# Performance work log

Hardware: AMD Instinct MI355X
Metric: run time of the kernel (lower is better)

The kernel has to match this reference:

```python
import jax, jax.numpy as jnp
import numpy as np

N, F_IN, HID, NCLS, E = 50000, 128, 256, 40, 600000
BN_EPS = 1e-5


def setup_inputs() -> dict:
    key = jax.random.key(0)
    ks = jax.random.split(key, 12)
    x = jax.random.normal(ks[0], (N, F_IN), dtype=jnp.float32)
    edge_index = jax.random.randint(ks[1], (2, E), 0, N, dtype=jnp.int64)
    # BatchNorm0 (over input features) running stats + affine params
    bn0_gamma = jnp.ones((F_IN,), jnp.float32)
    bn0_beta = jnp.zeros((F_IN,), jnp.float32)
    bn0_mean = jax.random.normal(ks[2], (F_IN,), jnp.float32) * 0.1
    bn0_var = jax.random.uniform(ks[3], (F_IN,), jnp.float32, 0.5, 1.5)
    # GINConv1 linear: F_IN -> HID
    W1 = jax.random.normal(ks[4], (F_IN, HID), jnp.float32) / np.sqrt(F_IN)
    b1 = jnp.zeros((HID,), jnp.float32)
    # BatchNorm1 (over hidden)
    bn1_gamma = jnp.ones((HID,), jnp.float32)
    bn1_beta = jnp.zeros((HID,), jnp.float32)
    bn1_mean = jax.random.normal(ks[5], (HID,), jnp.float32) * 0.1
    bn1_var = jax.random.uniform(ks[6], (HID,), jnp.float32, 0.5, 1.5)
    # GINConv2 linear: HID -> NCLS
    W2 = jax.random.normal(ks[7], (HID, NCLS), jnp.float32) / np.sqrt(HID)
    b2 = jnp.zeros((NCLS,), jnp.float32)
    return {
        "x": x, "edge_index": edge_index,
        "bn0_gamma": bn0_gamma, "bn0_beta": bn0_beta,
        "bn0_mean": bn0_mean, "bn0_var": bn0_var,
        "W1": W1, "b1": b1,
        "bn1_gamma": bn1_gamma, "bn1_beta": bn1_beta,
        "bn1_mean": bn1_mean, "bn1_var": bn1_var,
        "W2": W2, "b2": b2,
    }


def _bn_eval(h, gamma, beta, mean, var):
    return (h - mean) * (gamma / jnp.sqrt(var + BN_EPS)) + beta


def _gin_agg(h, src, dst, n):
    # sum_{j in N(i)} h_j  (scatter-add over edges), plus self term (eps=0)
    return h + jax.ops.segment_sum(h[src], dst, num_segments=n)


def reference(x, edge_index, bn0_gamma, bn0_beta, bn0_mean, bn0_var,
              W1, b1, bn1_gamma, bn1_beta, bn1_mean, bn1_var, W2, b2):
    # Eval mode: dropout / dropout_edge are identity; BN uses running stats.
    src, dst = edge_index[0], edge_index[1]
    n = x.shape[0]
    h = _bn_eval(x, bn0_gamma, bn0_beta, bn0_mean, bn0_var)
    h = _gin_agg(h, src, dst, n) @ W1 + b1          # GINConv1
    h = _bn_eval(h, bn1_gamma, bn1_beta, bn1_mean, bn1_var)
    h = jax.nn.relu(h)
    out = _gin_agg(h, src, dst, n) @ W2 + b2        # GINConv2 -> logits [N, NCLS]
    return out
```

## Files before the change

kernel.cpp:

```cpp
#include <hip/hip_runtime.h>

#define NN 50000
#define FIN 128
#define HID 256
#define NCLS 40
#define NE 600000
#define BN_EPS 1e-5f
#define MAXDEG 64
#define GSTR 64
#define NSLICE 6250
#define NFILLB 4688
#define NCONVB 6250

typedef _Float16 half4_t __attribute__((ext_vector_type(4)));
typedef _Float16 half8_t __attribute__((ext_vector_type(8)));
typedef float float2_t __attribute__((ext_vector_type(2)));
typedef float float4_t __attribute__((ext_vector_type(4)));


#define OFF_DEG    1600000
#define OFF_GH     1664000
#define OFF_XQ     3264000
#define OFF_W1T    4864000
#define OFF_W2T    4880384
#define OFF_P      4886528
#define OFF_Q      4886784

__global__ void prep_convert_fill_k(const float* __restrict__ W1, const float* __restrict__ W2,
                                    const float* __restrict__ bn0_g, const float* __restrict__ bn0_b,
                                    const float* __restrict__ bn0_m, const float* __restrict__ bn0_v,
                                    const float* __restrict__ b1,
                                    const float* __restrict__ bn1_g, const float* __restrict__ bn1_b,
                                    const float* __restrict__ bn1_m, const float* __restrict__ bn1_v,
                                    _Float16* __restrict__ W1T, _Float16* __restrict__ W2T,
                                    float* __restrict__ p, float* __restrict__ q,
                                    const float4* __restrict__ x4, unsigned int* __restrict__ xq,
                                    const int* __restrict__ ei, int* __restrict__ deg,
                                    unsigned short* __restrict__ pad) {
    int t = threadIdx.x;
    int b = blockIdx.x;
    if (b >= 9) {
        int fb = b - 9;
        if (fb < NFILLB) {
            int grp = fb >> 3;
            int slice = fb & 7;
            int ebase = grp * 1024 + t;
            #pragma unroll
            for (int k = 0; k < 4; ++k) {
                int e = ebase + k * 256;
                if (e < NE) {
                    int dst = ei[NE + e];
                    if (dst / NSLICE == slice) {
                        int src = ei[e];
                        int pos = atomicAdd(&deg[dst], 1);
                        if (pos < MAXDEG) pad[(size_t)dst * MAXDEG + pos] = (unsigned short)src;
                    }
                }
            }
        } else {
            int i = (fb - NFILLB) * 256 + t;
            if (i < NN * 32) {
                float4 v = x4[i];
                int r = 0;
                r = __builtin_amdgcn_cvt_pk_fp8_f32(v.x, v.y, r, false);
                r = __builtin_amdgcn_cvt_pk_fp8_f32(v.z, v.w, r, true);
                xq[i] = (unsigned int)r;
            }
        }
        return;
    }
    if (b < 8) {
        __shared__ _Float16 T[64][65];
        __shared__ float s0l[64], s1l[64];
        int k0 = (b >> 2) * 64;
        int c0 = (b & 3) * 64;
        if (t < 64) {
            s0l[t] = bn0_g[k0 + t] * rsqrtf(bn0_v[k0 + t] + BN_EPS);
        } else if (t < 128) {
            int c = t - 64;
            s1l[c] = bn1_g[c0 + c] * rsqrtf(bn1_v[c0 + c] + BN_EPS);
        }
        __syncthreads();
        int cc = t & 63;
        #pragma unroll
        for (int i = 0; i < 16; ++i) {
            int idx = i * 256 + t;
            int kk = idx >> 6;
            T[cc][kk] = (_Float16)(W1[(size_t)(k0 + kk) * HID + c0 + cc] * s0l[kk] * s1l[cc]);
        }
        __syncthreads();
        #pragma unroll
        for (int i = 0; i < 16; ++i) {
            int idx = i * 256 + t;
            int c2 = idx >> 6, kk2 = idx & 63;
            W1T[(size_t)(c0 + c2) * FIN + k0 + kk2] = T[c2][kk2];
        }
    } else {
        __shared__ float t0s[FIN];
        if (t < FIN) {
            float s = bn0_g[t] * rsqrtf(bn0_v[t] + BN_EPS);
            t0s[t] = bn0_b[t] - bn0_m[t] * s;
        }
        float sc = bn1_g[t] * rsqrtf(bn1_v[t] + BN_EPS);
        __syncthreads();
        float v = 0.f;
        for (int k = 0; k < FIN; ++k) v += t0s[k] * W1[(size_t)k * HID + t];
        p[t] = v * sc;
        q[t] = (b1[t] - bn1_m[t]) * sc + bn1_b[t];
        for (int c = 0; c < 48; ++c) {
            float w = (c < NCLS) ? W2[(size_t)t * NCLS + c] : 0.f;
            W2T[(size_t)c * HID + t] = (_Float16)w;
        }
    }
}

#define FP8ACC(v)                                                          \
    {                                                                      \
        float2_t f0 = __builtin_amdgcn_cvt_pk_f32_fp8((int)(v).x, false);  \
        float2_t f1 = __builtin_amdgcn_cvt_pk_f32_fp8((int)(v).x, true);   \
        float2_t f2 = __builtin_amdgcn_cvt_pk_f32_fp8((int)(v).y, false);  \
        float2_t f3 = __builtin_amdgcn_cvt_pk_f32_fp8((int)(v).y, true);   \
        ax0 += f0[0]; ax1 += f0[1]; ax2 += f1[0]; ax3 += f1[1];            \
        ax4 += f2[0]; ax5 += f2[1]; ax6 += f3[0]; ax7 += f3[1];            \
    }

__launch_bounds__(256, 6)
__global__ void gather_gemm_k(const uint2* __restrict__ xq, const int* __restrict__ deg,
                              const unsigned short* __restrict__ pad,
                              const _Float16* __restrict__ W1T, const _Float16* __restrict__ W2T,
                              const float* __restrict__ p, const float* __restrict__ q,
                              _Float16* __restrict__ gh) {
    __shared__ _Float16 smem[32 * 264];
    __shared__ float scdeg[32];
    int t = threadIdx.x;
    int w = t >> 6, lane = t & 63;
    int l16 = lane & 15;
    int qw = lane >> 4;
    int sbase = lane & 48;
    int node_base = blockIdx.x * 32;

    for (int pr = 0; pr < 2; ++pr) {
        int ln = w * 8 + pr * 4 + qw;
        int n = node_base + ln;
        float ax0 = 0.f, ax1 = 0.f, ax2 = 0.f, ax3 = 0.f;
        float ax4 = 0.f, ax5 = 0.f, ax6 = 0.f, ax7 = 0.f;
        int dcnt = 0;
        if (n < NN) {
            int d = deg[n];
            dcnt = d < MAXDEG ? d : MAXDEG;
            uint2 sv = xq[(size_t)n * 16 + l16];
            FP8ACC(sv);
        }
        int base = 0;
        while (base < dcnt) {
            int cnt = dcnt - base;
            if (cnt > 16) cnt = 16;
            int vi = (l16 < cnt) ? (int)pad[(size_t)n * MAXDEG + base + l16] : 0;
            int j = 0;
            for (; j + 7 < cnt; j += 8) {
                int s0 = __shfl(vi, sbase + j),     s1 = __shfl(vi, sbase + j + 1);
                int s2 = __shfl(vi, sbase + j + 2), s3 = __shfl(vi, sbase + j + 3);
                int s4 = __shfl(vi, sbase + j + 4), s5 = __shfl(vi, sbase + j + 5);
                int s6 = __shfl(vi, sbase + j + 6), s7 = __shfl(vi, sbase + j + 7);
                uint2 v0 = xq[(size_t)s0 * 16 + l16];
                uint2 v1 = xq[(size_t)s1 * 16 + l16];
                uint2 v2 = xq[(size_t)s2 * 16 + l16];
                uint2 v3 = xq[(size_t)s3 * 16 + l16];
                uint2 v4 = xq[(size_t)s4 * 16 + l16];
                uint2 v5 = xq[(size_t)s5 * 16 + l16];
                uint2 v6 = xq[(size_t)s6 * 16 + l16];
                uint2 v7 = xq[(size_t)s7 * 16 + l16];
                FP8ACC(v0); FP8ACC(v1); FP8ACC(v2); FP8ACC(v3);
                FP8ACC(v4); FP8ACC(v5); FP8ACC(v6); FP8ACC(v7);
            }
            for (; j + 3 < cnt; j += 4) {
                int s0 = __shfl(vi, sbase + j),     s1 = __shfl(vi, sbase + j + 1);
                int s2 = __shfl(vi, sbase + j + 2), s3 = __shfl(vi, sbase + j + 3);
                uint2 v0 = xq[(size_t)s0 * 16 + l16];
                uint2 v1 = xq[(size_t)s1 * 16 + l16];
                uint2 v2 = xq[(size_t)s2 * 16 + l16];
                uint2 v3 = xq[(size_t)s3 * 16 + l16];
                FP8ACC(v0); FP8ACC(v1); FP8ACC(v2); FP8ACC(v3);
            }
            for (; j < cnt; ++j) {
                int s = __shfl(vi, sbase + j);
                uint2 v = xq[(size_t)s * 16 + l16];
                FP8ACC(v);
            }
            base += 16;
        }
        half8_t o;
        o[0] = (_Float16)ax0; o[1] = (_Float16)ax1;
        o[2] = (_Float16)ax2; o[3] = (_Float16)ax3;
        o[4] = (_Float16)ax4; o[5] = (_Float16)ax5;
        o[6] = (_Float16)ax6; o[7] = (_Float16)ax7;
        *(half8_t*)&smem[ln * 136 + l16 * 8] = o;
        if (l16 == 0) scdeg[ln] = 1.0f + (float)dcnt;
    }
    __syncthreads();

    int l15 = lane & 15, quad = lane >> 4;
    half8_t a[2][4];
    #pragma unroll
    for (int nb = 0; nb < 2; ++nb)
        #pragma unroll
        for (int ks = 0; ks < 4; ++ks)
            a[nb][ks] = *(const half8_t*)&smem[(nb * 16 + l15) * 136 + ks * 32 + quad * 8];
    __syncthreads();

    #pragma unroll
    for (int ci = 0; ci < 4; ++ci) {
        int ct = w * 4 + ci;
        float4_t acc0 = {0.f, 0.f, 0.f, 0.f};
        float4_t acc1 = {0.f, 0.f, 0.f, 0.f};
        #pragma unroll
        for (int ks = 0; ks < 4; ++ks) {
            half8_t b = *(const half8_t*)(W1T + (size_t)(ct * 16 + l15) * FIN + ks * 32 + quad * 8);
            acc0 = __builtin_amdgcn_mfma_f32_16x16x32_f16(a[0][ks], b, acc0, 0, 0, 0);
            acc1 = __builtin_amdgcn_mfma_f32_16x16x32_f16(a[1][ks], b, acc1, 0, 0, 0);
        }
        int col = ct * 16 + l15;
        float pc = p[col], qc = q[col];
        #pragma unroll
        for (int r = 0; r < 4; ++r) {
            int row = quad * 4 + r;
            float h0 = acc0[r] + scdeg[row] * pc + qc;
            smem[row * 264 + col] = (_Float16)fmaxf(h0, 0.f);
            float h1 = acc1[r] + scdeg[16 + row] * pc + qc;
            smem[(16 + row) * 264 + col] = (_Float16)fmaxf(h1, 0.f);
        }
    }
    __syncthreads();

    for (int rep = 0; rep < 2; ++rep) {
        int tau = w + rep * 4;
        if (tau >= 6) break;
        int nb = tau / 3, ct2 = tau - nb * 3;
        half8_t a2[8];
        #pragma unroll
        for (int ks = 0; ks < 8; ++ks)
            a2[ks] = *(const half8_t*)&smem[(nb * 16 + l15) * 264 + ks * 32 + quad * 8];
        float4_t c = {0.f, 0.f, 0.f, 0.f};
        #pragma unroll
        for (int ks = 0; ks < 8; ++ks) {
            half8_t b = *(const half8_t*)(W2T + (size_t)(ct2 * 16 + l15) * HID + ks * 32 + quad * 8);
            c = __builtin_amdgcn_mfma_f32_16x16x32_f16(a2[ks], b, c, 0, 0, 0);
        }
        int col = ct2 * 16 + l15;
        #pragma unroll
        for (int r = 0; r < 4; ++r) {
            int n = node_base + nb * 16 + quad * 4 + r;
            if (n < NN) gh[(size_t)n * GSTR + col] = (_Float16)c[r];
        }
    }
}

__global__ void gather2_k(const _Float16* __restrict__ gh, const int* __restrict__ deg,
                          const unsigned short* __restrict__ pad, const float* __restrict__ b2,
                          float* __restrict__ out) {
    int gid = blockIdx.x * 256 + threadIdx.x;
    int n = gid >> 6, lane = gid & 63;
    if (n >= NN) return;
    int dcnt = deg[n];
    if (dcnt > MAXDEG) dcnt = MAXDEG;
    float acc = (float)gh[(size_t)n * GSTR + lane];
    int vi = (lane < dcnt) ? (int)pad[(size_t)n * MAXDEG + lane] : 0;
    int j = 0;
    for (; j + 7 < dcnt; j += 8) {
        int s0 = __shfl(vi, j),     s1 = __shfl(vi, j + 1);
        int s2 = __shfl(vi, j + 2), s3 = __shfl(vi, j + 3);
        int s4 = __shfl(vi, j + 4), s5 = __shfl(vi, j + 5);
        int s6 = __shfl(vi, j + 6), s7 = __shfl(vi, j + 7);
        float v0 = (float)gh[(size_t)s0 * GSTR + lane];
        float v1 = (float)gh[(size_t)s1 * GSTR + lane];
        float v2 = (float)gh[(size_t)s2 * GSTR + lane];
        float v3 = (float)gh[(size_t)s3 * GSTR + lane];
        float v4 = (float)gh[(size_t)s4 * GSTR + lane];
        float v5 = (float)gh[(size_t)s5 * GSTR + lane];
        float v6 = (float)gh[(size_t)s6 * GSTR + lane];
        float v7 = (float)gh[(size_t)s7 * GSTR + lane];
        acc += ((v0 + v1) + (v2 + v3)) + ((v4 + v5) + (v6 + v7));
    }
    for (; j + 3 < dcnt; j += 4) {
        int s0 = __shfl(vi, j),     s1 = __shfl(vi, j + 1);
        int s2 = __shfl(vi, j + 2), s3 = __shfl(vi, j + 3);
        acc += ((float)gh[(size_t)s0 * GSTR + lane] + (float)gh[(size_t)s1 * GSTR + lane])
             + ((float)gh[(size_t)s2 * GSTR + lane] + (float)gh[(size_t)s3 * GSTR + lane]);
    }
    for (; j < dcnt; ++j) {
        int s = __shfl(vi, j);
        acc += (float)gh[(size_t)s * GSTR + lane];
    }
    if (lane < NCLS) out[(size_t)n * NCLS + lane] = acc + b2[lane];
}

extern "C" void kernel_launch(void* const* d_in, const int* in_sizes, int n_in,
                              void* d_out, int out_size, void* d_ws, size_t ws_size,
                              hipStream_t stream) {
    const float* x      = (const float*)d_in[0];
    const int*   ei     = (const int*)d_in[1];
    const float* bn0_g  = (const float*)d_in[2];
    const float* bn0_b  = (const float*)d_in[3];
    const float* bn0_m  = (const float*)d_in[4];
    const float* bn0_v  = (const float*)d_in[5];
    const float* W1     = (const float*)d_in[6];
    const float* b1     = (const float*)d_in[7];
    const float* bn1_g  = (const float*)d_in[8];
    const float* bn1_b  = (const float*)d_in[9];
    const float* bn1_m  = (const float*)d_in[10];
    const float* bn1_v  = (const float*)d_in[11];
    const float* W2     = (const float*)d_in[12];
    const float* b2     = (const float*)d_in[13];
    float* out = (float*)d_out;

    float* ws = (float*)d_ws;
    int*   wi = (int*)d_ws;
    unsigned short* pad = (unsigned short*)d_ws;
    int* deg           = wi + OFF_DEG;
    _Float16* gh       = (_Float16*)(ws + OFF_GH);
    unsigned int* xq   = (unsigned int*)(ws + OFF_XQ);
    _Float16* W1T      = (_Float16*)(ws + OFF_W1T);
    _Float16* W2T      = (_Float16*)(ws + OFF_W2T);
    float* p           = ws + OFF_P;
    float* q           = ws + OFF_Q;

    hipMemsetAsync(deg, 0, NN * sizeof(int), stream);

    hipLaunchKernelGGL(prep_convert_fill_k,
                       dim3(9 + NFILLB + NCONVB), dim3(256), 0, stream,
                       W1, W2, bn0_g, bn0_b, bn0_m, bn0_v, b1,
                       bn1_g, bn1_b, bn1_m, bn1_v, W1T, W2T, p, q,
                       (const float4*)x, xq, ei, deg, pad);

    hipLaunchKernelGGL(gather_gemm_k, dim3((NN + 31) / 32), dim3(256), 0, stream,
                       (const uint2*)xq, deg, pad, W1T, W2T, p, q, gh);

    hipLaunchKernelGGL(gather2_k, dim3((NN * 64 + 255) / 256), dim3(256), 0, stream,
                       gh, deg, pad, b2, out);
}
```

Baseline: 189.9 us.

## Fuse three kernels into one persistent megakernel with grid barriers

Merges the prep/fill, gather+GEMM and second-gather kernels into a single persistent kernel of 768 blocks. Software grid barriers built on atomic counters replace kernel boundaries, and an atomic tile counter hands out GEMM tiles dynamically. The goal is to remove launch and drain gaps between stages. In exchange it caps resident waves at the persistent grid size, adds barrier spin cost, and depends on every block being co-resident to avoid deadlock.

```diff
diff --git a/kernel.cpp b/kernel.cpp
--- a/kernel.cpp
+++ b/kernel.cpp
@@ -11,14 +11,18 @@
 #define NSLICE 6250
 #define NFILLB 4688
 #define NCONVB 6250
-
-typedef _Float16 half4_t __attribute__((ext_vector_type(4)));
+#define NU1 (9 + NFILLB + NCONVB)
+#define NTILES 1563
+#define NU3 12500
+#define NBLK 768
+
 typedef _Float16 half8_t __attribute__((ext_vector_type(8)));
 typedef float float2_t __attribute__((ext_vector_type(2)));
 typedef float float4_t __attribute__((ext_vector_type(4)));
 
 
 #define OFF_DEG    1600000
+#define OFF_CTR    1650000
 #define OFF_GH     1664000
 #define OFF_XQ     3264000
 #define OFF_W1T    4864000
@@ -26,22 +30,100 @@
 #define OFF_P      4886528
 #define OFF_Q      4886784
 
-__global__ void prep_convert_fill_k(const float* __restrict__ W1, const float* __restrict__ W2,
-                                    const float* __restrict__ bn0_g, const float* __restrict__ bn0_b,
-                                    const float* __restrict__ bn0_m, const float* __restrict__ bn0_v,
-                                    const float* __restrict__ b1,
-                                    const float* __restrict__ bn1_g, const float* __restrict__ bn1_b,
-                                    const float* __restrict__ bn1_m, const float* __restrict__ bn1_v,
-                                    _Float16* __restrict__ W1T, _Float16* __restrict__ W2T,
-                                    float* __restrict__ p, float* __restrict__ q,
-                                    const float4* __restrict__ x4, unsigned int* __restrict__ xq,
-                                    const int* __restrict__ ei, int* __restrict__ deg,
-                                    unsigned short* __restrict__ pad) {
+#define FP8ACC(v)                                                          \
+    {                                                                      \
+        float2_t f0 = __builtin_amdgcn_cvt_pk_f32_fp8((int)(v).x, false);  \
+        float2_t f1 = __builtin_amdgcn_cvt_pk_f32_fp8((int)(v).x, true);   \
+        float2_t f2 = __builtin_amdgcn_cvt_pk_f32_fp8((int)(v).y, false);  \
+        float2_t f3 = __builtin_amdgcn_cvt_pk_f32_fp8((int)(v).y, true);   \
+        ax0 += f0[0]; ax1 += f0[1]; ax2 += f1[0]; ax3 += f1[1];            \
+        ax4 += f2[0]; ax5 += f2[1]; ax6 += f3[0]; ax7 += f3[1];            \
+    }
+
+__device__ __forceinline__ void grid_barrier(int* ctr, int target) {
+    __syncthreads();
+    if (threadIdx.x == 0) {
+        __hip_atomic_fetch_add(ctr, 1, __ATOMIC_RELEASE, __HIP_MEMORY_SCOPE_AGENT);
+        long spins = 0;
+        while (__hip_atomic_load(ctr, __ATOMIC_RELAXED, __HIP_MEMORY_SCOPE_AGENT) < target) {
+            __builtin_amdgcn_s_sleep(2);
+            if (++spins > 20000000L) break;
+        }
+        __hip_atomic_load(ctr, __ATOMIC_ACQUIRE, __HIP_MEMORY_SCOPE_AGENT);
+    }
+    __syncthreads();
+}
+
+__launch_bounds__(256, 6)
+__global__ void mega_k(const float* __restrict__ W1, const float* __restrict__ W2,
+                       const float* __restrict__ bn0_g, const float* __restrict__ bn0_b,
+                       const float* __restrict__ bn0_m, const float* __restrict__ bn0_v,
+                       const float* __restrict__ b1,
+                       const float* __restrict__ bn1_g, const float* __restrict__ bn1_b,
+                       const float* __restrict__ bn1_m, const float* __restrict__ bn1_v,
+                       const float4* __restrict__ x4, const int* __restrict__ ei,
+                       const float* __restrict__ b2, float* __restrict__ out,
+                       _Float16* __restrict__ W1T, _Float16* __restrict__ W2T,
+                       float* __restrict__ p, float* __restrict__ q,
+                       unsigned int* __restrict__ xq, int* __restrict__ deg,
+                       unsigned short* __restrict__ pad, _Float16* __restrict__ gh,
+                       int* __restrict__ ctr) {
+    __shared__ _Float16 smem[32 * 264];
+    __shared__ float scdeg[32];
+    __shared__ int sh_tile;
     int t = threadIdx.x;
     int b = blockIdx.x;
-    if (b >= 9) {
-        int fb = b - 9;
-        if (fb < NFILLB) {
+    int nb_grid = gridDim.x;
+    int w = t >> 6, lane = t & 63;
+
+    for (int u = b; u < NU1; u += nb_grid) {
+        if (u < 8) {
+            _Float16 (*T)[65] = (_Float16 (*)[65])smem;
+            float* s0l = (float*)(smem + 64 * 66);
+            float* s1l = s0l + 64;
+            int k0 = (u >> 2) * 64;
+            int c0 = (u & 3) * 64;
+            if (t < 64) {
+                s0l[t] = bn0_g[k0 + t] * rsqrtf(bn0_v[k0 + t] + BN_EPS);
+            } else if (t < 128) {
+                int c = t - 64;
+                s1l[c] = bn1_g[c0 + c] * rsqrtf(bn1_v[c0 + c] + BN_EPS);
+            }
+            __syncthreads();
+            int cc = t & 63;
+            #pragma unroll
+            for (int i = 0; i < 16; ++i) {
+                int idx = i * 256 + t;
+                int kk = idx >> 6;
+                T[cc][kk] = (_Float16)(W1[(size_t)(k0 + kk) * HID + c0 + cc] * s0l[kk] * s1l[cc]);
+            }
+            __syncthreads();
+            #pragma unroll
+            for (int i = 0; i < 16; ++i) {
+                int idx = i * 256 + t;
+                int c2 = idx >> 6, kk2 = idx & 63;
+                W1T[(size_t)(c0 + c2) * FIN + k0 + kk2] = T[c2][kk2];
+            }
+            __syncthreads();
+        } else if (u == 8) {
+            float* t0s = (float*)smem;
+            if (t < FIN) {
+                float s = bn0_g[t] * rsqrtf(bn0_v[t] + BN_EPS);
+                t0s[t] = bn0_b[t] - bn0_m[t] * s;
+            }
+            float sc = bn1_g[t] * rsqrtf(bn1_v[t] + BN_EPS);
+            __syncthreads();
+            float v = 0.f;
+            for (int k = 0; k < FIN; ++k) v += t0s[k] * W1[(size_t)k * HID + t];
+            p[t] = v * sc;
+            q[t] = (b1[t] - bn1_m[t]) * sc + bn1_b[t];
+            for (int c = 0; c < 48; ++c) {
+                float wv = (c < NCLS) ? W2[(size_t)t * NCLS + c] : 0.f;
+                W2T[(size_t)c * HID + t] = (_Float16)wv;
+            }
+            __syncthreads();
+        } else if (u < 9 + NFILLB) {
+            int fb = u - 9;
             int grp = fb >> 3;
             int slice = fb & 7;
             int ebase = grp * 1024 + t;
@@ -58,7 +140,7 @@
                 }
             }
         } else {
-            int i = (fb - NFILLB) * 256 + t;
+            int i = (u - 9 - NFILLB) * 256 + t;
             if (i < NN * 32) {
                 float4 v = x4[i];
                 int r = 0;
@@ -67,249 +149,191 @@
                 xq[i] = (unsigned int)r;
             }
         }
-        return;
-    }
-    if (b < 8) {
-        __shared__ _Float16 T[64][65];
-        __shared__ float s0l[64], s1l[64];
-        int k0 = (b >> 2) * 64;
-        int c0 = (b & 3) * 64;
-        if (t < 64) {
-            s0l[t] = bn0_g[k0 + t] * rsqrtf(bn0_v[k0 + t] + BN_EPS);
-        } else if (t < 128) {
-            int c = t - 64;
-            s1l[c] = bn1_g[c0 + c] * rsqrtf(bn1_v[c0 + c] + BN_EPS);
-        }
-        __syncthreads();
-        int cc = t & 63;
-        #pragma unroll
-        for (int i = 0; i < 16; ++i) {
-            int idx = i * 256 + t;
-            int kk = idx >> 6;
-            T[cc][kk] = (_Float16)(W1[(size_t)(k0 + kk) * HID + c0 + cc] * s0l[kk] * s1l[cc]);
-        }
-        __syncthreads();
-        #pragma unroll
-        for (int i = 0; i < 16; ++i) {
-            int idx = i * 256 + t;
-            int c2 = idx >> 6, kk2 = idx & 63;
-            W1T[(size_t)(c0 + c2) * FIN + k0 + kk2] = T[c2][kk2];
-        }
-    } else {
-        __shared__ float t0s[FIN];
-        if (t < FIN) {
-            float s = bn0_g[t] * rsqrtf(bn0_v[t] + BN_EPS);
-            t0s[t] = bn0_b[t] - bn0_m[t] * s;
-        }
-        float sc = bn1_g[t] * rsqrtf(bn1_v[t] + BN_EPS);
-        __syncthreads();
-        float v = 0.f;
-        for (int k = 0; k < FIN; ++k) v += t0s[k] * W1[(size_t)k * HID + t];
-        p[t] = v * sc;
-        q[t] = (b1[t] - bn1_m[t]) * sc + bn1_b[t];
-        for (int c = 0; c < 48; ++c) {
-            float w = (c < NCLS) ? W2[(size_t)t * NCLS + c] : 0.f;
-            W2T[(size_t)c * HID + t] = (_Float16)w;
-        }
-    }
-}
-
-#define FP8ACC(v)                                                          \
-    {                                                                      \
-        float2_t f0 = __builtin_amdgcn_cvt_pk_f32_fp8((int)(v).x, false);  \
-        float2_t f1 = __builtin_amdgcn_cvt_pk_f32_fp8((int)(v).x, true);   \
-        float2_t f2 = __builtin_amdgcn_cvt_pk_f32_fp8((int)(v).y, false);  \
-        float2_t f3 = __builtin_amdgcn_cvt_pk_f32_fp8((int)(v).y, true);   \
-        ax0 += f0[0]; ax1 += f0[1]; ax2 += f1[0]; ax3 += f1[1];            \
-        ax4 += f2[0]; ax5 += f2[1]; ax6 += f3[0]; ax7 += f3[1];            \
-    }
-
-__launch_bounds__(256, 6)
-__global__ void gather_gemm_k(const uint2* __restrict__ xq, const int* __restrict__ deg,
-                              const unsigned short* __restrict__ pad,
-                              const _Float16* __restrict__ W1T, const _Float16* __restrict__ W2T,
-                              const float* __restrict__ p, const float* __restrict__ q,
-                              _Float16* __restrict__ gh) {
-    __shared__ _Float16 smem[32 * 264];
-    __shared__ float scdeg[32];
-    int t = threadIdx.x;
-    int w = t >> 6, lane = t & 63;
+    }
+    grid_barrier(&ctr[0], nb_grid);
+
+    const uint2* xq2 = (const uint2*)xq;
     int l16 = lane & 15;
     int qw = lane >> 4;
     int sbase = lane & 48;
-    int node_base = blockIdx.x * 32;
-
-    for (int pr = 0; pr < 2; ++pr) {
-        int ln = w * 8 + pr * 4 + qw;
-        int n = node_base + ln;
-        float ax0 = 0.f, ax1 = 0.f, ax2 = 0.f, ax3 = 0.f;
-        float ax4 = 0.f, ax5 = 0.f, ax6 = 0.f, ax7 = 0.f;
-        int dcnt = 0;
-        if (n < NN) {
-            int d = deg[n];
-            dcnt = d < MAXDEG ? d : MAXDEG;
-            uint2 sv = xq[(size_t)n * 16 + l16];
-            FP8ACC(sv);
-        }
-        int base = 0;
-        while (base < dcnt) {
-            int cnt = dcnt - base;
-            if (cnt > 16) cnt = 16;
-            int vi = (l16 < cnt) ? (int)pad[(size_t)n * MAXDEG + base + l16] : 0;
-            int j = 0;
-            for (; j + 7 < cnt; j += 8) {
-                int s0 = __shfl(vi, sbase + j),     s1 = __shfl(vi, sbase + j + 1);
-                int s2 = __shfl(vi, sbase + j + 2), s3 = __shfl(vi, sbase + j + 3);
-                int s4 = __shfl(vi, sbase + j + 4), s5 = __shfl(vi, sbase + j + 5);
-                int s6 = __shfl(vi, sbase + j + 6), s7 = __shfl(vi, sbase + j + 7);
-                uint2 v0 = xq[(size_t)s0 * 16 + l16];
-                uint2 v1 = xq[(size_t)s1 * 16 + l16];
-                uint2 v2 = xq[(size_t)s2 * 16 + l16];
-                uint2 v3 = xq[(size_t)s3 * 16 + l16];
-                uint2 v4 = xq[(size_t)s4 * 16 + l16];
-                uint2 v5 = xq[(size_t)s5 * 16 + l16];
-                uint2 v6 = xq[(size_t)s6 * 16 + l16];
-                uint2 v7 = xq[(size_t)s7 * 16 + l16];
-                FP8ACC(v0); FP8ACC(v1); FP8ACC(v2); FP8ACC(v3);
-                FP8ACC(v4); FP8ACC(v5); FP8ACC(v6); FP8ACC(v7);
-            }
-            for (; j + 3 < cnt; j += 4) {
-                int s0 = __shfl(vi, sbase + j),     s1 = __shfl(vi, sbase + j + 1);
-                int s2 = __shfl(vi, sbase + j + 2), s3 = __shfl(vi, sbase + j + 3);
-                uint2 v0 = xq[(size_t)s0 * 16 + l16];
-                uint2 v1 = xq[(size_t)s1 * 16 + l16];
-                uint2 v2 = xq[(size_t)s2 * 16 + l16];
-                uint2 v3 = xq[(size_t)s3 * 16 + l16];
-                FP8ACC(v0); FP8ACC(v1); FP8ACC(v2); FP8ACC(v3);
-            }
-            for (; j < cnt; ++j) {
-                int s = __shfl(vi, sbase + j);
-                uint2 v = xq[(size_t)s * 16 + l16];
-                FP8ACC(v);
-            }
-            base += 16;
-        }
-        half8_t o;
-        o[0] = (_Float16)ax0; o[1] = (_Float16)ax1;
-        o[2] = (_Float16)ax2; o[3] = (_Float16)ax3;
-        o[4] = (_Float16)ax4; o[5] = (_Float16)ax5;
-        o[6] = (_Float16)ax6; o[7] = (_Float16)ax7;
-        *(half8_t*)&smem[ln * 136 + l16 * 8] = o;
-        if (l16 == 0) scdeg[ln] = 1.0f + (float)dcnt;
-    }
-    __syncthreads();
-
     int l15 = lane & 15, quad = lane >> 4;
-    half8_t a[2][4];
-    #pragma unroll
-    for (int nb = 0; nb < 2; ++nb)
+    for (;;) {
+        __syncthreads();
+        if (t == 0) sh_tile = atomicAdd(&ctr[2], 1);
+        __syncthreads();
+        int tile = sh_tile;
+        if (tile >= NTILES) break;
+        int node_base = tile * 32;
+
+        for (int pr = 0; pr < 2; ++pr) {
+            int ln = w * 8 + pr * 4 + qw;
+            int n = node_base + ln;
+            float ax0 = 0.f, ax1 = 0.f, ax2 = 0.f, ax3 = 0.f;
+            float ax4 = 0.f, ax5 = 0.f, ax6 = 0.f, ax7 = 0.f;
+            int dcnt = 0;
+            if (n < NN) {
+                int d = deg[n];
+                dcnt = d < MAXDEG ? d : MAXDEG;
+                uint2 sv = xq2[(size_t)n * 16 + l16];
+                FP8ACC(sv);
+            }
+            int base = 0;
+            while (base < dcnt) {
+                int cnt = dcnt - base;
+                if (cnt > 16) cnt = 16;
+                int vi = (l16 < cnt) ? (int)pad[(size_t)n * MAXDEG + base + l16] : 0;
+                int j = 0;
+                for (; j + 7 < cnt; j += 8) {
+                    int s0 = __shfl(vi, sbase + j),     s1 = __shfl(vi, sbase + j + 1);
+                    int s2 = __shfl(vi, sbase + j + 2), s3 = __shfl(vi, sbase + j + 3);
+                    int s4 = __shfl(vi, sbase + j + 4), s5 = __shfl(vi, sbase + j + 5);
+                    int s6 = __shfl(vi, sbase + j + 6), s7 = __shfl(vi, sbase + j + 7);
+                    uint2 v0 = xq2[(size_t)s0 * 16 + l16];
+                    uint2 v1 = xq2[(size_t)s1 * 16 + l16];
+                    uint2 v2 = xq2[(size_t)s2 * 16 + l16];
+                    uint2 v3 = xq2[(size_t)s3 * 16 + l16];
+                    uint2 v4 = xq2[(size_t)s4 * 16 + l16];
+                    uint2 v5 = xq2[(size_t)s5 * 16 + l16];
+                    uint2 v6 = xq2[(size_t)s6 * 16 + l16];
+                    uint2 v7 = xq2[(size_t)s7 * 16 + l16];
+                    FP8ACC(v0); FP8ACC(v1); FP8ACC(v2); FP8ACC(v3);
+                    FP8ACC(v4); FP8ACC(v5); FP8ACC(v6); FP8ACC(v7);
+                }
+                for (; j + 3 < cnt; j += 4) {
+                    int s0 = __shfl(vi, sbase + j),     s1 = __shfl(vi, sbase + j + 1);
+                    int s2 = __shfl(vi, sbase + j + 2), s3 = __shfl(vi, sbase + j + 3);
+                    uint2 v0 = xq2[(size_t)s0 * 16 + l16];
+                    uint2 v1 = xq2[(size_t)s1 * 16 + l16];
+                    uint2 v2 = xq2[(size_t)s2 * 16 + l16];
+                    uint2 v3 = xq2[(size_t)s3 * 16 + l16];
+                    FP8ACC(v0); FP8ACC(v1); FP8ACC(v2); FP8ACC(v3);
+                }
+                for (; j < cnt; ++j) {
+                    int s = __shfl(vi, sbase + j);
+                    uint2 v = xq2[(size_t)s * 16 + l16];
+                    FP8ACC(v);
+                }
+                base += 16;
+            }
+            half8_t o;
+            o[0] = (_Float16)ax0; o[1] = (_Float16)ax1;
+            o[2] = (_Float16)ax2; o[3] = (_Float16)ax3;
+            o[4] = (_Float16)ax4; o[5] = (_Float16)ax5;
+            o[6] = (_Float16)ax6; o[7] = (_Float16)ax7;
+            *(half8_t*)&smem[ln * 136 + l16 * 8] = o;
+            if (l16 == 0) scdeg[ln] = 1.0f + (float)dcnt;
+        }
+        __syncthreads();
+
+        half8_t a[2][4];
         #pragma unroll
-        for (int ks = 0; ks < 4; ++ks)
-            a[nb][ks] = *(const half8_t*)&smem[(nb * 16 + l15) * 136 + ks * 32 + quad * 8];
-    __syncthreads();
-
-    #pragma unroll
-    for (int ci = 0; ci < 4; ++ci) {
-        int ct = w * 4 + ci;
-        float4_t acc0 = {0.f, 0.f, 0.f, 0.f};
-        float4_t acc1 = {0.f, 0.f, 0.f, 0.f};
+        for (int nb = 0; nb < 2; ++nb)
+            #pragma unroll
+            for (int ks = 0; ks < 4; ++ks)
+                a[nb][ks] = *(const half8_t*)&smem[(nb * 16 + l15) * 136 + ks * 32 + quad * 8];
+        __syncthreads();
+
         #pragma unroll
-        for (int ks = 0; ks < 4; ++ks) {
-            half8_t b = *(const half8_t*)(W1T + (size_t)(ct * 16 + l15) * FIN + ks * 32 + quad * 8);
-            acc0 = __builtin_amdgcn_mfma_f32_16x16x32_f16(a[0][ks], b, acc0, 0, 0, 0);
-            acc1 = __builtin_amdgcn_mfma_f32_16x16x32_f16(a[1][ks], b, acc1, 0, 0, 0);
-        }
-        int col = ct * 16 + l15;
-        float pc = p[col], qc = q[col];
-        #pragma unroll
-        for (int r = 0; r < 4; ++r) {
-            int row = quad * 4 + r;
-            float h0 = acc0[r] + scdeg[row] * pc + qc;
-            smem[row * 264 + col] = (_Float16)fmaxf(h0, 0.f);
-            float h1 = acc1[r] + scdeg[16 + row] * pc + qc;
-            smem[(16 + row) * 264 + col] = (_Float16)fmaxf(h1, 0.f);
-        }
-    }
-    __syncthreads();
-
-    for (int rep = 0; rep < 2; ++rep) {
-        int tau = w + rep * 4;
-        if (tau >= 6) break;
-        int nb = tau / 3, ct2 = tau - nb * 3;
-        half8_t a2[8];
-        #pragma unroll
-        for (int ks = 0; ks < 8; ++ks)
-            a2[ks] = *(const half8_t*)&smem[(nb * 16 + l15) * 264 + ks * 32 + quad * 8];
-        float4_t c = {0.f, 0.f, 0.f, 0.f};
-        #pragma unroll
-        for (int ks = 0; ks < 8; ++ks) {
-            half8_t b = *(const half8_t*)(W2T + (size_t)(ct2 * 16 + l15) * HID + ks * 32 + quad * 8);
-            c = __builtin_amdgcn_mfma_f32_16x16x32_f16(a2[ks], b, c, 0, 0, 0);
-        }
-        int col = ct2 * 16 + l15;
-        #pragma unroll
-        for (int r = 0; r < 4; ++r) {
-            int n = node_base + nb * 16 + quad * 4 + r;
-            if (n < NN) gh[(size_t)n * GSTR + col] = (_Float16)c[r];
-        }
-    }
-}
-
-__global__ void gather2_k(const _Float16* __restrict__ gh, const int* __restrict__ deg,
-                          const unsigned short* __restrict__ pad, const float* __restrict__ b2,
-                          float* __restrict__ out) {
-    int gid = blockIdx.x * 256 + threadIdx.x;
-    int n = gid >> 6, lane = gid & 63;
-    if (n >= NN) return;
-    int dcnt = deg[n];
-    if (dcnt > MAXDEG) dcnt = MAXDEG;
-    float acc = (float)gh[(size_t)n * GSTR + lane];
-    int vi = (lane < dcnt) ? (int)pad[(size_t)n * MAXDEG + lane] : 0;
-    int j = 0;
-    for (; j + 7 < dcnt; j += 8) {
-        int s0 = __shfl(vi, j),     s1 = __shfl(vi, j + 1);
-        int s2 = __shfl(vi, j + 2), s3 = __shfl(vi, j + 3);
-        int s4 = __shfl(vi, j + 4), s5 = __shfl(vi, j + 5);
-        int s6 = __shfl(vi, j + 6), s7 = __shfl(vi, j + 7);
-        float v0 = (float)gh[(size_t)s0 * GSTR + lane];
-        float v1 = (float)gh[(size_t)s1 * GSTR + lane];
-        float v2 = (float)gh[(size_t)s2 * GSTR + lane];
-        float v3 = (float)gh[(size_t)s3 * GSTR + lane];
-        float v4 = (float)gh[(size_t)s4 * GSTR + lane];
-        float v5 = (float)gh[(size_t)s5 * GSTR + lane];
-        float v6 = (float)gh[(size_t)s6 * GSTR + lane];
-        float v7 = (float)gh[(size_t)s7 * GSTR + lane];
-        acc += ((v0 + v1) + (v2 + v3)) + ((v4 + v5) + (v6 + v7));
-    }
-    for (; j + 3 < dcnt; j += 4) {
-        int s0 = __shfl(vi, j),     s1 = __shfl(vi, j + 1);
-        int s2 = __shfl(vi, j + 2), s3 = __shfl(vi, j + 3);
-        acc += ((float)gh[(size_t)s0 * GSTR + lane] + (float)gh[(size_t)s1 * GSTR + lane])
-             + ((float)gh[(size_t)s2 * GSTR + lane] + (float)gh[(size_t)s3 * GSTR + lane]);
-    }
-    for (; j < dcnt; ++j) {
-        int s = __shfl(vi, j);
-        acc += (float)gh[(size_t)s * GSTR + lane];
-    }
-    if (lane < NCLS) out[(size_t)n * NCLS + lane] = acc + b2[lane];
+        for (int ci = 0; ci < 4; ++ci) {
+            int ct = w * 4 + ci;
+            float4_t acc0 = {0.f, 0.f, 0.f, 0.f};
+            float4_t acc1 = {0.f, 0.f, 0.f, 0.f};
+            #pragma unroll
+            for (int ks = 0; ks < 4; ++ks) {
+                half8_t bb = *(const half8_t*)(W1T + (size_t)(ct * 16 + l15) * FIN + ks * 32 + quad * 8);
+                acc0 = __builtin_amdgcn_mfma_f32_16x16x32_f16(a[0][ks], bb, acc0, 0, 0, 0);
+                acc1 = __builtin_amdgcn_mfma_f32_16x16x32_f16(a[1][ks], bb, acc1, 0, 0, 0);
+            }
+            int col = ct * 16 + l15;
+            float pc = p[col], qc = q[col];
+            #pragma unroll
+            for (int r = 0; r < 4; ++r) {
+                int row = quad * 4 + r;
+                float h0 = acc0[r] + scdeg[row] * pc + qc;
+                smem[row * 264 + col] = (_Float16)fmaxf(h0, 0.f);
+                float h1 = acc1[r] + scdeg[16 + row] * pc + qc;
+                smem[(16 + row) * 264 + col] = (_Float16)fmaxf(h1, 0.f);
+            }
+        }
+        __syncthreads();
+
+        for (int rep = 0; rep < 2; ++rep) {
+            int tau = w + rep * 4;
+            if (tau >= 6) break;
+            int nb = tau / 3, ct2 = tau - nb * 3;
+            half8_t a2[8];
+            #pragma unroll
+            for (int ks = 0; ks < 8; ++ks)
+                a2[ks] = *(const half8_t*)&smem[(nb * 16 + l15) * 264 + ks * 32 + quad * 8];
+            float4_t c = {0.f, 0.f, 0.f, 0.f};
+            #pragma unroll
+            for (int ks = 0; ks < 8; ++ks) {
+                half8_t bb = *(const half8_t*)(W2T + (size_t)(ct2 * 16 + l15) * HID + ks * 32 + quad * 8);
+                c = __builtin_amdgcn_mfma_f32_16x16x32_f16(a2[ks], bb, c, 0, 0, 0);
+            }
+            int col = ct2 * 16 + l15;
+            #pragma unroll
+            for (int r = 0; r < 4; ++r) {
+                int n = node_base + nb * 16 + quad * 4 + r;
+                if (n < NN) gh[(size_t)n * GSTR + col] = (_Float16)c[r];
+            }
+        }
+    }
+    grid_barrier(&ctr[1], nb_grid);
+
+    for (int u = b; u < NU3; u += nb_grid) {
+        int n = u * 4 + w;
+        if (n >= NN) continue;
+        int dcnt = deg[n];
+        if (dcnt > MAXDEG) dcnt = MAXDEG;
+        float acc = (float)gh[(size_t)n * GSTR + lane];
+        int vi = (lane < dcnt) ? (int)pad[(size_t)n * MAXDEG + lane] : 0;
+        int j = 0;
+        for (; j + 7 < dcnt; j += 8) {
+            int s0 = __shfl(vi, j),     s1 = __shfl(vi, j + 1);
+            int s2 = __shfl(vi, j + 2), s3 = __shfl(vi, j + 3);
+            int s4 = __shfl(vi, j + 4), s5 = __shfl(vi, j + 5);
+            int s6 = __shfl(vi, j + 6), s7 = __shfl(vi, j + 7);
+            float v0 = (float)gh[(size_t)s0 * GSTR + lane];
+            float v1 = (float)gh[(size_t)s1 * GSTR + lane];
+            float v2 = (float)gh[(size_t)s2 * GSTR + lane];
+            float v3 = (float)gh[(size_t)s3 * GSTR + lane];
+            float v4 = (float)gh[(size_t)s4 * GSTR + lane];
+            float v5 = (float)gh[(size_t)s5 * GSTR + lane];
+            float v6 = (float)gh[(size_t)s6 * GSTR + lane];
+            float v7 = (float)gh[(size_t)s7 * GSTR + lane];
+            acc += ((v0 + v1) + (v2 + v3)) + ((v4 + v5) + (v6 + v7));
+        }
+        for (; j + 3 < dcnt; j += 4) {
+            int s0 = __shfl(vi, j),     s1 = __shfl(vi, j + 1);
+            int s2 = __shfl(vi, j + 2), s3 = __shfl(vi, j + 3);
+            acc += ((float)gh[(size_t)s0 * GSTR + lane] + (float)gh[(size_t)s1 * GSTR + lane])
+                 + ((float)gh[(size_t)s2 * GSTR + lane] + (float)gh[(size_t)s3 * GSTR + lane]);
+        }
+        for (; j < dcnt; ++j) {
+            int s = __shfl(vi, j);
+            acc += (float)gh[(size_t)s * GSTR + lane];
+        }
+        if (lane < NCLS) out[(size_t)n * NCLS + lane] = acc + b2[lane];
+    }
 }
 
 extern "C" void kernel_launch(void* const* d_in, const int* in_sizes, int n_in,
                               void* d_out, int out_size, void* d_ws, size_t ws_size,
                               hipStream_t stream) {
-    const float* x      = (const float*)d_in[0];
-    const int*   ei     = (const int*)d_in[1];
+    const float* W1     = (const float*)d_in[6];
+    const float* W2     = (const float*)d_in[12];
     const float* bn0_g  = (const float*)d_in[2];
     const float* bn0_b  = (const float*)d_in[3];
     const float* bn0_m  = (const float*)d_in[4];
     const float* bn0_v  = (const float*)d_in[5];
-    const float* W1     = (const float*)d_in[6];
     const float* b1     = (const float*)d_in[7];
     const float* bn1_g  = (const float*)d_in[8];
     const float* bn1_b  = (const float*)d_in[9];
     const float* bn1_m  = (const float*)d_in[10];
     const float* bn1_v  = (const float*)d_in[11];
-    const float* W2     = (const float*)d_in[12];
+    const float4* x4    = (const float4*)d_in[0];
+    const int*   ei     = (const int*)d_in[1];
     const float* b2     = (const float*)d_in[13];
     float* out = (float*)d_out;
 
@@ -317,6 +341,7 @@
     int*   wi = (int*)d_ws;
     unsigned short* pad = (unsigned short*)d_ws;
     int* deg           = wi + OFF_DEG;
+    int* ctr           = wi + OFF_CTR;
     _Float16* gh       = (_Float16*)(ws + OFF_GH);
     unsigned int* xq   = (unsigned int*)(ws + OFF_XQ);
     _Float16* W1T      = (_Float16*)(ws + OFF_W1T);
@@ -324,17 +349,11 @@
     float* p           = ws + OFF_P;
     float* q           = ws + OFF_Q;
 
-    hipMemsetAsync(deg, 0, NN * sizeof(int), stream);
-
-    hipLaunchKernelGGL(prep_convert_fill_k,
-                       dim3(9 + NFILLB + NCONVB), dim3(256), 0, stream,
+    hipMemsetAsync(deg, 0, (size_t)(NN + 3) * sizeof(int), stream);
+
+    hipLaunchKernelGGL(mega_k, dim3(NBLK), dim3(256), 0, stream,
                        W1, W2, bn0_g, bn0_b, bn0_m, bn0_v, b1,
-                       bn1_g, bn1_b, bn1_m, bn1_v, W1T, W2T, p, q,
-                       (const float4*)x, xq, ei, deg, pad);
-
-    hipLaunchKernelGGL(gather_gemm_k, dim3((NN + 31) / 32), dim3(256), 0, stream,
-                       (const uint2*)xq, deg, pad, W1T, W2T, p, q, gh);
-
-    hipLaunchKernelGGL(gather2_k, dim3((NN * 64 + 255) / 256), dim3(256), 0, stream,
-                       gh, deg, pad, b2, out);
+                       bn1_g, bn1_b, bn1_m, bn1_v,
+                       x4, ei, b2, out,
+                       W1T, W2T, p, q, xq, deg, pad, gh, ctr);
 }
```

After: 471.9 us. +148.5%, slower.

## Process four nodes per wavefront in layer-2 gather with 8-byte vector loads

Applied to the files above, without the earlier changes.

The second-layer gather now assigns 16 lanes per node, so each wavefront handles four nodes. Each lane loads four fp16 features at once as a uint2, which replaces one 2-byte load per lane over 64 lanes, most of them padding beyond the 40 classes. Neighbor indices are fetched in chunks of 16 and broadcast within each quarter-wave by shuffles. This cuts wasted lanes and load instructions. The cost is more divergence, because the four nodes in a wave have different degrees, and the final output is written as strided scalar stores.

```diff
diff --git a/kernel.cpp b/kernel.cpp
--- a/kernel.cpp
+++ b/kernel.cpp
@@ -255,43 +255,79 @@
     }
 }
 
-__global__ void gather2_k(const _Float16* __restrict__ gh, const int* __restrict__ deg,
+__global__ void gather2_k(const uint2* __restrict__ gh2, const int* __restrict__ deg,
                           const unsigned short* __restrict__ pad, const float* __restrict__ b2,
                           float* __restrict__ out) {
     int gid = blockIdx.x * 256 + threadIdx.x;
-    int n = gid >> 6, lane = gid & 63;
+    int wid = gid >> 6;
+    int lane = gid & 63;
+    int l16 = lane & 15;
+    int qw = lane >> 4;
+    int sbase = lane & 48;
+    int n = wid * 4 + qw;
     if (n >= NN) return;
+
     int dcnt = deg[n];
     if (dcnt > MAXDEG) dcnt = MAXDEG;
-    float acc = (float)gh[(size_t)n * GSTR + lane];
-    int vi = (lane < dcnt) ? (int)pad[(size_t)n * MAXDEG + lane] : 0;
-    int j = 0;
-    for (; j + 7 < dcnt; j += 8) {
-        int s0 = __shfl(vi, j),     s1 = __shfl(vi, j + 1);
-        int s2 = __shfl(vi, j + 2), s3 = __shfl(vi, j + 3);
-        int s4 = __shfl(vi, j + 4), s5 = __shfl(vi, j + 5);
-        int s6 = __shfl(vi, j + 6), s7 = __shfl(vi, j + 7);
-        float v0 = (float)gh[(size_t)s0 * GSTR + lane];
-        float v1 = (float)gh[(size_t)s1 * GSTR + lane];
-        float v2 = (float)gh[(size_t)s2 * GSTR + lane];
-        float v3 = (float)gh[(size_t)s3 * GSTR + lane];
-        float v4 = (float)gh[(size_t)s4 * GSTR + lane];
-        float v5 = (float)gh[(size_t)s5 * GSTR + lane];
-        float v6 = (float)gh[(size_t)s6 * GSTR + lane];
-        float v7 = (float)gh[(size_t)s7 * GSTR + lane];
-        acc += ((v0 + v1) + (v2 + v3)) + ((v4 + v5) + (v6 + v7));
-    }
-    for (; j + 3 < dcnt; j += 4) {
-        int s0 = __shfl(vi, j),     s1 = __shfl(vi, j + 1);
-        int s2 = __shfl(vi, j + 2), s3 = __shfl(vi, j + 3);
-        acc += ((float)gh[(size_t)s0 * GSTR + lane] + (float)gh[(size_t)s1 * GSTR + lane])
-             + ((float)gh[(size_t)s2 * GSTR + lane] + (float)gh[(size_t)s3 * GSTR + lane]);
-    }
-    for (; j < dcnt; ++j) {
-        int s = __shfl(vi, j);
-        acc += (float)gh[(size_t)s * GSTR + lane];
-    }
-    if (lane < NCLS) out[(size_t)n * NCLS + lane] = acc + b2[lane];
+
+    float ax0, ax1, ax2, ax3;
+    {
+        half4_t sv = *(const half4_t*)&gh2[(size_t)n * 16 + l16];
+        ax0 = (float)sv[0]; ax1 = (float)sv[1]; ax2 = (float)sv[2]; ax3 = (float)sv[3];
+    }
+#define GHACC(v)                                                     \
+    {                                                                \
+        half4_t hv = *(half4_t*)&(v);                                \
+        ax0 += (float)hv[0]; ax1 += (float)hv[1];                    \
+        ax2 += (float)hv[2]; ax3 += (float)hv[3];                    \
+    }
+    int base = 0;
+    while (base < dcnt) {
+        int cnt = dcnt - base;
+        if (cnt > 16) cnt = 16;
+        int vi = (l16 < cnt) ? (int)pad[(size_t)n * MAXDEG + base + l16] : 0;
+        int j = 0;
+        for (; j + 7 < cnt; j += 8) {
+            int s0 = __shfl(vi, sbase + j),     s1 = __shfl(vi, sbase + j + 1);
+            int s2 = __shfl(vi, sbase + j + 2), s3 = __shfl(vi, sbase + j + 3);
+            int s4 = __shfl(vi, sbase + j + 4), s5 = __shfl(vi, sbase + j + 5);
+            int s6 = __shfl(vi, sbase + j + 6), s7 = __shfl(vi, sbase + j + 7);
+            uint2 v0 = gh2[(size_t)s0 * 16 + l16];
+            uint2 v1 = gh2[(size_t)s1 * 16 + l16];
+            uint2 v2 = gh2[(size_t)s2 * 16 + l16];
+            uint2 v3 = gh2[(size_t)s3 * 16 + l16];
+            uint2 v4 = gh2[(size_t)s4 * 16 + l16];
+            uint2 v5 = gh2[(size_t)s5 * 16 + l16];
+            uint2 v6 = gh2[(size_t)s6 * 16 + l16];
+            uint2 v7 = gh2[(size_t)s7 * 16 + l16];
+            GHACC(v0); GHACC(v1); GHACC(v2); GHACC(v3);
+            GHACC(v4); GHACC(v5); GHACC(v6); GHACC(v7);
+        }
+        for (; j + 3 < cnt; j += 4) {
+            int s0 = __shfl(vi, sbase + j),     s1 = __shfl(vi, sbase + j + 1);
+            int s2 = __shfl(vi, sbase + j + 2), s3 = __shfl(vi, sbase + j + 3);
+            uint2 v0 = gh2[(size_t)s0 * 16 + l16];
+            uint2 v1 = gh2[(size_t)s1 * 16 + l16];
+            uint2 v2 = gh2[(size_t)s2 * 16 + l16];
+            uint2 v3 = gh2[(size_t)s3 * 16 + l16];
+            GHACC(v0); GHACC(v1); GHACC(v2); GHACC(v3);
+        }
+        for (; j < cnt; ++j) {
+            int s = __shfl(vi, sbase + j);
+            uint2 v = gh2[(size_t)s * 16 + l16];
+            GHACC(v);
+        }
+        base += 16;
+    }
+#undef GHACC
+    int c0 = l16 * 4;
+    if (c0 < NCLS) {
+        float* op = &out[(size_t)n * NCLS + c0];
+        op[0] = ax0 + b2[c0];
+        op[1] = ax1 + b2[c0 + 1];
+        op[2] = ax2 + b2[c0 + 2];
+        op[3] = ax3 + b2[c0 + 3];
+    }
 }
 
 extern "C" void kernel_launch(void* const* d_in, const int* in_sizes, int n_in,
@@ -335,6 +371,6 @@
     hipLaunchKernelGGL(gather_gemm_k, dim3((NN + 31) / 32), dim3(256), 0, stream,
                        (const uint2*)xq, deg, pad, W1T, W2T, p, q, gh);
 
-    hipLaunchKernelGGL(gather2_k, dim3((NN * 64 + 255) / 256), dim3(256), 0, stream,
-                       gh, deg, pad, b2, out);
+    hipLaunchKernelGGL(gather2_k, dim3(3125), dim3(256), 0, stream,
+                       (const uint2*)gh, deg, pad, b2, out);
 }
```

Result: no change. 189.4 us (-0.2%).
